# Performance work log

Measured on AMD Instinct MI355X. Metric: run time of the kernel, lower is better.

Reference implementation:

```python
import jax, jax.numpy as jnp
import numpy as np

B, T, D, H = 4, 2048, 1024, 16
HS = D // H

def _layernorm(x, g, b, eps=1e-5):
    mu = jnp.mean(x, axis=-1, keepdims=True)
    var = jnp.var(x, axis=-1, keepdims=True)
    return (x - mu) * jax.lax.rsqrt(var + eps) * g + b

def setup_inputs() -> dict:
    key = jax.random.key(0)
    ks = jax.random.split(key, 8)
    s = 0.02
    return {
        "x": jax.random.normal(ks[0], (B, T, D), jnp.float32),
        "wq": jax.random.normal(ks[1], (D, D), jnp.float32) * s,
        "wk": jax.random.normal(ks[2], (D, D), jnp.float32) * s,
        "wv": jax.random.normal(ks[3], (D, D), jnp.float32) * s,
        "wo": jax.random.normal(ks[4], (D, D), jnp.float32) * s,
        "bo": jnp.zeros((D,), jnp.float32),
        "w1": jax.random.normal(ks[5], (D, 4 * D), jnp.float32) * s,
        "b1": jnp.zeros((4 * D,), jnp.float32),
        "w2": jax.random.normal(ks[6], (4 * D, D), jnp.float32) * s,
        "b2": jnp.zeros((D,), jnp.float32),
        "g1": jnp.ones((D,), jnp.float32),
        "be1": jnp.zeros((D,), jnp.float32),
        "g2": jnp.ones((D,), jnp.float32),
        "be2": jnp.zeros((D,), jnp.float32),
    }

def reference(x, wq, wk, wv, wo, bo, w1, b1, w2, b2, g1, be1, g2, be2):
    b, t, d = x.shape
    h = H
    hs = d // h
    # --- pre-LN + multi-head causal self-attention ---
    xn = _layernorm(x, g1, be1)
    q = (xn @ wq).reshape(b, t, h, hs).transpose(0, 2, 1, 3)  # [b,h,t,hs]
    k = (xn @ wk).reshape(b, t, h, hs).transpose(0, 2, 1, 3)
    v = (xn @ wv).reshape(b, t, h, hs).transpose(0, 2, 1, 3)
    # NOTE: original scales by C**-0.5 where C = embedded_size (not head_size)
    scale = jnp.asarray(d, x.dtype) ** -0.5
    wei = jnp.einsum("bhqd,bhkd->bhqk", q, k) * scale
    causal = jnp.tril(jnp.ones((t, t), bool))
    wei = jnp.where(causal, wei, -jnp.inf)
    wei = jax.nn.softmax(wei, axis=-1)
    attn = jnp.einsum("bhqk,bhkd->bhqd", wei, v)
    attn = attn.transpose(0, 2, 1, 3).reshape(b, t, d)
    x = x + attn @ wo + bo
    # --- pre-LN + FFN ---
    xn2 = _layernorm(x, g2, be2)
    x = x + jax.nn.relu(xn2 @ w1 + b1) @ w2 + b2
    return x
```

## Files before the change

### kernel.cpp

```cpp
#include <hip/hip_runtime.h>
#include <hip/hip_bf16.h>
#include <stdint.h>

typedef __hip_bfloat16 bf16;
typedef __attribute__((ext_vector_type(8))) short bf16x8_t;
typedef __attribute__((ext_vector_type(4))) float f32x4_t;
typedef __attribute__((ext_vector_type(16))) float f32x16_t;
typedef __attribute__((ext_vector_type(2))) unsigned int u32x2_t;

#define B_ 4
#define T_ 2048
#define D_ 1024
#define H_ 16
#define HS_ 64
#define QKV_LD 3072

__device__ __forceinline__ void gload_lds16(const void* g, void* l) {
    __builtin_amdgcn_global_load_lds(
        (const __attribute__((address_space(1))) unsigned int*)g,
        (__attribute__((address_space(3))) unsigned int*)l, 16, 0, 0);
}

__device__ __forceinline__ bf16x8_t ldsv8(const bf16* p) {
    return *(const bf16x8_t*)p;
}

__device__ __forceinline__ unsigned pack2(float a, float b) {
    union { bf16 h[2]; unsigned u; } t;
    t.h[0] = __float2bfloat16(a);
    t.h[1] = __float2bfloat16(b);
    return t.u;
}

__global__ __launch_bounds__(256) void transpose_cvt(
    const float* __restrict__ W, bf16* __restrict__ WT, int K, int N)
{
    __shared__ float tile[32][33];
    const int nbx = N >> 5;
    const int bx = blockIdx.x % nbx;
    const int by = blockIdx.x / nbx;
    const int n0 = bx << 5, k0 = by << 5;
    const int tx = threadIdx.x & 31, ty = threadIdx.x >> 5;
#pragma unroll
    for (int i = 0; i < 32; i += 8)
        tile[ty + i][tx] = W[(long)(k0 + ty + i) * N + n0 + tx];
    __syncthreads();
#pragma unroll
    for (int i = 0; i < 32; i += 8)
        WT[(long)(n0 + ty + i) * K + k0 + tx] = __float2bfloat16(tile[tx][ty + i]);
}

__global__ __launch_bounds__(256) void vhead_transpose(
    const bf16* __restrict__ QKV, bf16* __restrict__ VT)
{
    __shared__ bf16 tile[32][33];
    int idx = blockIdx.x;
    const int tt  = idx & 63;   idx >>= 6;
    const int hst = idx & 1;    idx >>= 1;
    const int bh  = idx;
    const int b = bh >> 4, h = bh & 15;
    const int tx = threadIdx.x & 31, ty = threadIdx.x >> 5;
    const long vrow = (long)b * T_ + tt * 32;
    const int  vcol = 2048 + h * HS_ + hst * 32;
#pragma unroll
    for (int i = 0; i < 32; i += 8)
        tile[ty + i][tx] = QKV[(vrow + ty + i) * QKV_LD + vcol + tx];
    __syncthreads();
    const long orow = (long)bh * HS_ + hst * 32;
#pragma unroll
    for (int i = 0; i < 32; i += 8)
        VT[(orow + ty + i) * T_ + tt * 32 + tx] = tile[tx][ty + i];
}

__global__ __launch_bounds__(256) void ln_k(
    const float* __restrict__ x, const float* __restrict__ g,
    const float* __restrict__ be, bf16* __restrict__ out)
{
    const long row = blockIdx.x;
    const int t = threadIdx.x;
    const float4 v = ((const float4*)(x + row * D_))[t];
    float s  = v.x + v.y + v.z + v.w;
    float s2 = v.x * v.x + v.y * v.y + v.z * v.z + v.w * v.w;
#pragma unroll
    for (int m = 1; m < 64; m <<= 1) {
        s  += __shfl_xor(s, m, 64);
        s2 += __shfl_xor(s2, m, 64);
    }
    __shared__ float red[8];
    const int wv = t >> 6, ln = t & 63;
    if (ln == 0) { red[wv] = s; red[4 + wv] = s2; }
    __syncthreads();
    s  = red[0] + red[1] + red[2] + red[3];
    s2 = red[4] + red[5] + red[6] + red[7];
    const float mu  = s * (1.f / (float)D_);
    const float var = s2 * (1.f / (float)D_) - mu * mu;
    const float rs  = rsqrtf(var + 1e-5f);
    const float4 gv = ((const float4*)g)[t];
    const float4 bv = ((const float4*)be)[t];
    union { bf16 h[4]; short4 s4; } u;
    u.h[0] = __float2bfloat16((v.x - mu) * rs * gv.x + bv.x);
    u.h[1] = __float2bfloat16((v.y - mu) * rs * gv.y + bv.y);
    u.h[2] = __float2bfloat16((v.z - mu) * rs * gv.z + bv.z);
    u.h[3] = __float2bfloat16((v.w - mu) * rs * gv.w + bv.w);
    ((short4*)(out + row * D_))[t] = u.s4;
}

template<int HAS_BIAS, int RELU, int HAS_RES, int OUT_BF16>
__global__ __launch_bounds__(512, 1) void gemm2(
    const bf16* __restrict__ A, const bf16* __restrict__ BT,
    const float* __restrict__ bias, const float* __restrict__ res,
    void* __restrict__ Cout, int M, int N, int K)
{
    __shared__ bf16 As[2][256 * 64];
    __shared__ bf16 Bs[2][128 * 64];
    const int tid  = threadIdx.x;
    const int w    = tid >> 6;
    const int lane = tid & 63;
    const int wm = w >> 1, wn = w & 1;
    const int nbn = N >> 7;
    const int cpx = gridDim.x >> 3;
    const int bid = (blockIdx.x & 7) * cpx + (blockIdx.x >> 3);
    const int bm = bid / nbn, bn = bid % nbn;
    const int row0 = bm << 8, col0 = bn << 7;

    const bf16* aS0; const bf16* aS1; const bf16* aS2; const bf16* aS3;
    const bf16* bS0; const bf16* bS1;
    {
        int f0 = tid,        r0 = f0 >> 3, c0 = ((f0 & 7) ^ (r0 & 7)) << 3;
        int f1 = 512 + tid,  r1 = f1 >> 3, c1 = ((f1 & 7) ^ (r1 & 7)) << 3;
        int f2 = 1024 + tid, r2 = f2 >> 3, c2 = ((f2 & 7) ^ (r2 & 7)) << 3;
        int f3 = 1536 + tid, r3 = f3 >> 3, c3 = ((f3 & 7) ^ (r3 & 7)) << 3;
        aS0 = A + (long)(row0 + r0) * K + c0;
        aS1 = A + (long)(row0 + r1) * K + c1;
        aS2 = A + (long)(row0 + r2) * K + c2;
        aS3 = A + (long)(row0 + r3) * K + c3;
        bS0 = BT + (long)(col0 + r0) * K + c0;
        bS1 = BT + (long)(col0 + r1) * K + c1;
    }
    const int wbase = w * 64;

#define STAGE2(buf, kt) do {                                             \
        const long ko_ = (long)(kt) * 64;                                \
        gload_lds16(aS0 + ko_, &As[buf][(0 * 512 + wbase) * 8]);         \
        gload_lds16(aS1 + ko_, &As[buf][(1 * 512 + wbase) * 8]);         \
        gload_lds16(aS2 + ko_, &As[buf][(2 * 512 + wbase) * 8]);         \
        gload_lds16(aS3 + ko_, &As[buf][(3 * 512 + wbase) * 8]);         \
        gload_lds16(bS0 + ko_, &Bs[buf][(0 * 512 + wbase) * 8]);         \
        gload_lds16(bS1 + ko_, &Bs[buf][(1 * 512 + wbase) * 8]);         \
    } while (0)

    f32x4_t acc[4][4] = {};
    const int fr = lane & 15;
    const int fq = lane >> 4;
    const int nt = K >> 6;

    STAGE2(0, 0);
    STAGE2(1, 1);

    for (int t = 0; t < nt; ++t) {
        const int cur = t & 1;
        if (t < nt - 1) asm volatile("s_waitcnt vmcnt(6)" ::: "memory");
        else            asm volatile("s_waitcnt vmcnt(0)" ::: "memory");
        __builtin_amdgcn_s_barrier();

        bf16x8_t a[2][4], b[2][4];
#pragma unroll
        for (int ks = 0; ks < 2; ++ks) {
#pragma unroll
            for (int m = 0; m < 4; ++m) {
                const int r = wm * 64 + m * 16 + fr;
                const int ch = ks * 4 + fq;
                a[ks][m] = ldsv8(&As[cur][r * 64 + ((ch ^ (r & 7)) << 3)]);
            }
#pragma unroll
            for (int n = 0; n < 4; ++n) {
                const int r = wn * 64 + n * 16 + fr;
                const int ch = ks * 4 + fq;
                b[ks][n] = ldsv8(&Bs[cur][r * 64 + ((ch ^ (r & 7)) << 3)]);
            }
        }
        asm volatile("s_waitcnt lgkmcnt(0)" ::: "memory");
        __builtin_amdgcn_sched_barrier(0);
        __builtin_amdgcn_s_barrier();

        if (t + 2 < nt) STAGE2(cur, t + 2);

        __builtin_amdgcn_s_setprio(1);
#pragma unroll
        for (int m = 0; m < 4; ++m)
#pragma unroll
            for (int n = 0; n < 4; ++n) {
                acc[m][n] = __builtin_amdgcn_mfma_f32_16x16x32_bf16(a[0][m], b[0][n], acc[m][n], 0, 0, 0);
                acc[m][n] = __builtin_amdgcn_mfma_f32_16x16x32_bf16(a[1][m], b[1][n], acc[m][n], 0, 0, 0);
            }
        __builtin_amdgcn_s_setprio(0);
    }
#undef STAGE2

    const int orow = fq << 2;
#pragma unroll
    for (int m = 0; m < 4; ++m) {
        const int rbase = row0 + wm * 64 + m * 16 + orow;
#pragma unroll
        for (int n = 0; n < 4; ++n) {
            const int c = col0 + wn * 64 + n * 16 + fr;
            float bv = 0.f;
            if (HAS_BIAS) bv = bias[c];
#pragma unroll
            for (int r = 0; r < 4; ++r) {
                float v = acc[m][n][r] + bv;
                if (RELU) v = fmaxf(v, 0.f);
                if (HAS_RES) v += res[(long)(rbase + r) * N + c];
                if (OUT_BF16)
                    ((bf16*)Cout)[(long)(rbase + r) * N + c] = __float2bfloat16(v);
                else
                    ((float*)Cout)[(long)(rbase + r) * N + c] = v;
            }
        }
    }
}

template<int HAS_BIAS, int RELU, int HAS_RES, int OUT_BF16>
__global__ __launch_bounds__(512, 1) void gemm8(
    const bf16* __restrict__ A, const bf16* __restrict__ BT,
    const float* __restrict__ bias, const float* __restrict__ res,
    void* __restrict__ Cout, int M, int N, int K)
{
    __shared__ bf16 As[2][2][256 * 32];
    __shared__ bf16 Bs[2][2][256 * 32];

    const int tid  = threadIdx.x;
    const int w    = tid >> 6;
    const int lane = tid & 63;
    const int wm = w >> 2, wn = w & 3;
    const int nbn = N >> 8;
    const int cpx = gridDim.x >> 3;
    const int bid = (blockIdx.x & 7) * cpx + (blockIdx.x >> 3);
    const int bm = bid / nbn, bn = bid % nbn;
    const int row0 = bm << 8, col0 = bn << 8;

    const int r0s = tid >> 2;
    const int c0s = (((tid & 3) ^ (r0s & 3)) << 3);
    const bf16* aU0 = A  + (long)(row0 + r0s) * K + c0s;
    const bf16* aU1 = aU0 + (long)128 * K;
    const bf16* bU0 = BT + (long)(col0 + r0s) * K + c0s;
    const bf16* bU1 = bU0 + (long)128 * K;
    const int wb8 = w * 64 * 8;

#define STAGE_A8(buf, kh, kt) do {                                        \
        const long ko_ = (long)(kt) * 64 + (kh) * 32;                     \
        gload_lds16(aU0 + ko_, &As[buf][kh][wb8]);                        \
        gload_lds16(aU1 + ko_, &As[buf][kh][4096 + wb8]);                 \
    } while (0)
#define STAGE_B8(buf, kh, kt) do {                                        \
        const long ko_ = (long)(kt) * 64 + (kh) * 32;                     \
        gload_lds16(bU0 + ko_, &Bs[buf][kh][wb8]);                        \
        gload_lds16(bU1 + ko_, &Bs[buf][kh][4096 + wb8]);                 \
    } while (0)

    f32x4_t acc[8][4] = {};
    bf16x8_t af[8], bf0, bf1;
    const int fr = lane & 15;
    const int fq = lane >> 4;
    const int nt = K >> 6;

#define RD_A8(cur, ks) do { _Pragma("unroll")                              \
        for (int m = 0; m < 8; ++m) {                                      \
            const int rr = wm * 128 + m * 16 + fr;                         \
            af[m] = ldsv8(&As[cur][ks][rr * 32 + ((fq ^ (rr & 3)) << 3)]); \
        } } while (0)
#define RD_B8(cur, ks, n) ldsv8(&Bs[cur][ks][(wn * 64 + (n) * 16 + fr) * 32 + \
        ((fq ^ ((wn * 64 + (n) * 16 + fr) & 3)) << 3)])
#define MM8(nh) do { _Pragma("unroll")                                     \
        for (int m = 0; m < 8; ++m) {                                      \
            acc[m][(nh)*2]   = __builtin_amdgcn_mfma_f32_16x16x32_bf16(af[m], bf0, acc[m][(nh)*2],   0, 0, 0); \
            acc[m][(nh)*2+1] = __builtin_amdgcn_mfma_f32_16x16x32_bf16(af[m], bf1, acc[m][(nh)*2+1], 0, 0, 0); \
        } } while (0)
#define PHASE8(cur, ks, nh, RDA, STG, VM) do {                             \
        if (RDA) RD_A8(cur, ks);                                           \
        bf0 = RD_B8(cur, ks, (nh) * 2);                                    \
        bf1 = RD_B8(cur, ks, (nh) * 2 + 1);                                \
        STG;                                                               \
        __builtin_amdgcn_s_barrier();                                      \
        asm volatile("s_waitcnt lgkmcnt(0)" ::: "memory");                 \
        __builtin_amdgcn_sched_barrier(0);                                 \
        __builtin_amdgcn_s_setprio(1);                                     \
        MM8(nh);                                                           \
        __builtin_amdgcn_s_setprio(0);                                     \
        VM;                                                                \
        __builtin_amdgcn_s_barrier();                                      \
    } while (0)
#define VM4_ asm volatile("s_waitcnt vmcnt(4)" ::: "memory")
#define VM0_ asm volatile("s_waitcnt vmcnt(0)" ::: "memory")

    STAGE_A8(0, 0, 0);
    STAGE_B8(0, 0, 0);
    STAGE_A8(0, 1, 0);
    STAGE_B8(0, 1, 0);
    VM4_;
    __builtin_amdgcn_s_barrier();

    for (int t = 0; t < nt - 1; ++t) {
        const int cur = t & 1, nb = cur ^ 1;
        PHASE8(cur, 0, 0, 1, STAGE_A8(nb, 0, t + 1), (void)0);
        PHASE8(cur, 0, 1, 0, STAGE_B8(nb, 0, t + 1), VM4_);
        PHASE8(cur, 1, 0, 1, STAGE_A8(nb, 1, t + 1), (void)0);
        PHASE8(cur, 1, 1, 0, STAGE_B8(nb, 1, t + 1), VM4_);
    }
    {
        const int cur = (nt - 1) & 1;
        PHASE8(cur, 0, 0, 1, (void)0, (void)0);
        PHASE8(cur, 0, 1, 0, (void)0, VM0_);
        PHASE8(cur, 1, 0, 1, (void)0, (void)0);
        PHASE8(cur, 1, 1, 0, (void)0, (void)0);
    }
#undef STAGE_A8
#undef STAGE_B8
#undef RD_A8
#undef RD_B8
#undef MM8
#undef PHASE8
#undef VM4_
#undef VM0_

    const int orow = fq << 2;
#pragma unroll
    for (int m = 0; m < 8; ++m) {
        const int rbase = row0 + wm * 128 + m * 16 + orow;
#pragma unroll
        for (int n = 0; n < 4; ++n) {
            const int c = col0 + wn * 64 + n * 16 + fr;
            float bv = 0.f;
            if (HAS_BIAS) bv = bias[c];
#pragma unroll
            for (int r = 0; r < 4; ++r) {
                float v = acc[m][n][r] + bv;
                if (RELU) v = fmaxf(v, 0.f);
                if (HAS_RES) v += res[(long)(rbase + r) * N + c];
                if (OUT_BF16)
                    ((bf16*)Cout)[(long)(rbase + r) * N + c] = __float2bfloat16(v);
                else
                    ((float*)Cout)[(long)(rbase + r) * N + c] = v;
            }
        }
    }
}

__device__ __forceinline__ void attn_tile(
    const bf16* K_, const bf16* V_, const bf16x8_t (&qf)[4],
    f32x16_t& oA, f32x16_t& oB, float& mOld, float& lSum,
    int c, int ct_w, int qabs, int w, int l31, int hi, int hi8, int swzk)
{
    const float kE  = 0.0450842200278f;
    const float THR = 256.0f;
    const bool diag = (c == ct_w);
    const bool two  = !(diag && !(w & 1));

    f32x16_t s0 = {}, s1 = {};
#pragma unroll
    for (int s = 0; s < 4; ++s) {
        bf16x8_t kf = ldsv8(K_ + l31 * 64 + ((16 * s + hi8) ^ swzk));
        s0 = __builtin_amdgcn_mfma_f32_32x32x16_bf16(kf, qf[s], s0, 0, 0, 0);
    }
    if (two) {
#pragma unroll
        for (int s = 0; s < 4; ++s) {
            bf16x8_t kf = ldsv8(K_ + (32 + l31) * 64 + ((16 * s + hi8) ^ swzk));
            s1 = __builtin_amdgcn_mfma_f32_32x32x16_bf16(kf, qf[s], s1, 0, 0, 0);
        }
    }

    if (diag) {
        const int stm = w & 1;
        const int kb0 = c * 64 + stm * 32 + 4 * hi;
        if (stm) {
#pragma unroll
            for (int r = 0; r < 16; ++r)
                if (kb0 + (r & 3) + 8 * (r >> 2) > qabs) s1[r] = -1e30f;
        } else {
#pragma unroll
            for (int r = 0; r < 16; ++r)
                if (kb0 + (r & 3) + 8 * (r >> 2) > qabs) s0[r] = -1e30f;
        }
    }

    float rm = s0[0];
#pragma unroll
    for (int r = 1; r < 16; ++r) rm = fmaxf(rm, s0[r]);
    if (two) {
#pragma unroll
        for (int r = 0; r < 16; ++r) rm = fmaxf(rm, s1[r]);
    }
    {
        u32x2_t rr = __builtin_amdgcn_permlane32_swap(
            __float_as_uint(rm), __float_as_uint(rm), false, false);
        rm = fmaxf(__uint_as_float(rr.x), __uint_as_float(rr.y));
    }
    if (!__all(rm <= mOld + THR)) {
        const float mN = fmaxf(mOld, rm);
        const float corr = exp2f((mOld - mN) * kE);
#pragma unroll
        for (int r = 0; r < 16; ++r) { oA[r] *= corr; oB[r] *= corr; }
        lSum *= corr;
        mOld = mN;
    }
    const float nmk = -mOld * kE;
#pragma unroll
    for (int r = 0; r < 16; ++r) s0[r] = exp2f(fmaf(s0[r], kE, nmk));
    if (two) {
#pragma unroll
        for (int r = 0; r < 16; ++r) s1[r] = exp2f(fmaf(s1[r], kE, nmk));
    }
    float rs = s0[0];
#pragma unroll
    for (int r = 1; r < 16; ++r) rs += s0[r];
    if (two) {
#pragma unroll
        for (int r = 0; r < 16; ++r) rs += s1[r];
    }
    {
        u32x2_t rr = __builtin_amdgcn_permlane32_swap(
            __float_as_uint(rs), __float_as_uint(rs), false, false);
        rs = __uint_as_float(rr.x) + __uint_as_float(rr.y);
    }
    lSum += rs;

    {
        unsigned pk_[8];
#pragma unroll
        for (int i = 0; i < 8; ++i) pk_[i] = pack2(s0[2 * i], s0[2 * i + 1]);
        union { unsigned u[4]; bf16x8_t v; } W0, W1;
        u32x2_t ra = __builtin_amdgcn_permlane32_swap(pk_[0], pk_[2], false, false);
        u32x2_t rb = __builtin_amdgcn_permlane32_swap(pk_[1], pk_[3], false, false);
        W0.u[0] = ra.x; W0.u[1] = rb.x; W0.u[2] = ra.y; W0.u[3] = rb.y;
        u32x2_t rc = __builtin_amdgcn_permlane32_swap(pk_[4], pk_[6], false, false);
        u32x2_t rd = __builtin_amdgcn_permlane32_swap(pk_[5], pk_[7], false, false);
        W1.u[0] = rc.x; W1.u[1] = rd.x; W1.u[2] = rc.y; W1.u[3] = rd.y;
#pragma unroll
        for (int m = 0; m < 2; ++m) {
            const int kcol = 16 * m + hi8;
            bf16x8_t vf0 = ldsv8(V_ + l31 * 64 + (kcol ^ swzk));
            oA = __builtin_amdgcn_mfma_f32_32x32x16_bf16(vf0, m ? W1.v : W0.v, oA, 0, 0, 0);
            bf16x8_t vf1 = ldsv8(V_ + (32 + l31) * 64 + (kcol ^ swzk));
            oB = __builtin_amdgcn_mfma_f32_32x32x16_bf16(vf1, m ? W1.v : W0.v, oB, 0, 0, 0);
        }
    }
    if (two) {
        unsigned pk_[8];
#pragma unroll
        for (int i = 0; i < 8; ++i) pk_[i] = pack2(s1[2 * i], s1[2 * i + 1]);
        union { unsigned u[4]; bf16x8_t v; } W0, W1;
        u32x2_t ra = __builtin_amdgcn_permlane32_swap(pk_[0], pk_[2], false, false);
        u32x2_t rb = __builtin_amdgcn_permlane32_swap(pk_[1], pk_[3], false, false);
        W0.u[0] = ra.x; W0.u[1] = rb.x; W0.u[2] = ra.y; W0.u[3] = rb.y;
        u32x2_t rc = __builtin_amdgcn_permlane32_swap(pk_[4], pk_[6], false, false);
        u32x2_t rd = __builtin_amdgcn_permlane32_swap(pk_[5], pk_[7], false, false);
        W1.u[0] = rc.x; W1.u[1] = rd.x; W1.u[2] = rc.y; W1.u[3] = rd.y;
#pragma unroll
        for (int m = 0; m < 2; ++m) {
            const int kcol = 16 * (2 + m) + hi8;
            bf16x8_t vf0 = ldsv8(V_ + l31 * 64 + (kcol ^ swzk));
            oA = __builtin_amdgcn_mfma_f32_32x32x16_bf16(vf0, m ? W1.v : W0.v, oA, 0, 0, 0);
            bf16x8_t vf1 = ldsv8(V_ + (32 + l31) * 64 + (kcol ^ swzk));
            oB = __builtin_amdgcn_mfma_f32_32x32x16_bf16(vf1, m ? W1.v : W0.v, oB, 0, 0, 0);
        }
    }
}

__global__ __launch_bounds__(512, 1) void attn_flash(
    const bf16* __restrict__ QKV, const bf16* __restrict__ VT,
    bf16* __restrict__ O)
{
    __shared__ bf16 Ks[2][64 * 64];
    __shared__ bf16 Vs[2][64 * 64];

    const int tid = threadIdx.x;
    const int w   = tid >> 6;
    const int ln  = tid & 63;
    const int l31 = ln & 31;
    const int hi  = ln >> 5;
    const int hi8 = hi << 3;

    const int qLo = blockIdx.x;
    const int qHi = 7 - qLo;
    const int bh = blockIdx.y;
    const long rowBase = (long)(bh >> 4) * T_;
    const int colBase = (bh & 15) * HS_;

    const int qabsL = qLo * 256 + w * 32 + l31;
    const int qabsH = qHi * 256 + w * 32 + l31;
    const int ct_L  = qLo * 4 + (w >> 1);
    const int ct_H  = qHi * 4 + (w >> 1);
    const int ctb   = qHi * 4 + 3;

    bf16x8_t qfL[4], qfH[4];
    {
        const bf16* qpL = QKV + (rowBase + qabsL) * QKV_LD + colBase + hi8;
        const bf16* qpH = QKV + (rowBase + qabsH) * QKV_LD + colBase + hi8;
#pragma unroll
        for (int s = 0; s < 4; ++s) {
            qfL[s] = *(const bf16x8_t*)(qpL + 16 * s);
            qfH[s] = *(const bf16x8_t*)(qpH + 16 * s);
        }
    }

    f32x16_t oLA = {}, oLB = {}, oHA = {}, oHB = {};
    float mL = -1e30f, lL = 0.f, mH = -1e30f, lH = 0.f;

    const int srow = tid >> 3;
    const int schunk = (((tid & 7) ^ (srow & 7)) << 3);
    const bf16* kSrc = QKV + (rowBase + srow) * QKV_LD + 1024 + colBase + schunk;
    const bf16* vSrc = VT + ((long)bh * HS_ + srow) * T_ + schunk;

    gload_lds16(kSrc, &Ks[0][w * 512]);
    gload_lds16(vSrc, &Vs[0][w * 512]);

    const int swzk = (l31 & 7) << 3;

    for (int c = 0; c <= ctb; ++c) {
        const int cur = c & 1;
        __syncthreads();

        if (c < ctb) {
            gload_lds16(kSrc + (long)(c + 1) * 64 * QKV_LD, &Ks[cur ^ 1][w * 512]);
            gload_lds16(vSrc + (c + 1) * 64, &Vs[cur ^ 1][w * 512]);
        }

        const bf16* K_ = Ks[cur];
        const bf16* V_ = Vs[cur];
        if (c <= ct_H)
            attn_tile(K_, V_, qfH, oHA, oHB, mH, lH, c, ct_H, qabsH, w, l31, hi, hi8, swzk);
        if (c <= ct_L)
            attn_tile(K_, V_, qfL, oLA, oLB, mL, lL, c, ct_L, qabsL, w, l31, hi, hi8, swzk);
    }

    {
        const float inv = 1.f / lH;
        bf16* Op = O + (rowBase + qabsH) * D_ + colBase;
#pragma unroll
        for (int g = 0; g < 4; ++g) {
            u32x2_t sA, sB;
            sA.x = pack2(oHA[4 * g + 0] * inv, oHA[4 * g + 1] * inv);
            sA.y = pack2(oHA[4 * g + 2] * inv, oHA[4 * g + 3] * inv);
            sB.x = pack2(oHB[4 * g + 0] * inv, oHB[4 * g + 1] * inv);
            sB.y = pack2(oHB[4 * g + 2] * inv, oHB[4 * g + 3] * inv);
            *(u32x2_t*)(Op + 8 * g + 4 * hi)      = sA;
            *(u32x2_t*)(Op + 32 + 8 * g + 4 * hi) = sB;
        }
    }
    {
        const float inv = 1.f / lL;
        bf16* Op = O + (rowBase + qabsL) * D_ + colBase;
#pragma unroll
        for (int g = 0; g < 4; ++g) {
            u32x2_t sA, sB;
            sA.x = pack2(oLA[4 * g + 0] * inv, oLA[4 * g + 1] * inv);
            sA.y = pack2(oLA[4 * g + 2] * inv, oLA[4 * g + 3] * inv);
            sB.x = pack2(oLB[4 * g + 0] * inv, oLB[4 * g + 1] * inv);
            sB.y = pack2(oLB[4 * g + 2] * inv, oLB[4 * g + 3] * inv);
            *(u32x2_t*)(Op + 8 * g + 4 * hi)      = sA;
            *(u32x2_t*)(Op + 32 + 8 * g + 4 * hi) = sB;
        }
    }
}

extern "C" void kernel_launch(void* const* d_in, const int* in_sizes, int n_in,
                              void* d_out, int out_size, void* d_ws, size_t ws_size,
                              hipStream_t stream)
{
    (void)in_sizes; (void)n_in; (void)out_size; (void)ws_size;
    const float* x   = (const float*)d_in[0];
    const float* wq  = (const float*)d_in[1];
    const float* wk  = (const float*)d_in[2];
    const float* wv  = (const float*)d_in[3];
    const float* wo  = (const float*)d_in[4];
    const float* bo  = (const float*)d_in[5];
    const float* w1  = (const float*)d_in[6];
    const float* b1  = (const float*)d_in[7];
    const float* w2  = (const float*)d_in[8];
    const float* b2  = (const float*)d_in[9];
    const float* g1  = (const float*)d_in[10];
    const float* be1 = (const float*)d_in[11];
    const float* g2  = (const float*)d_in[12];
    const float* be2 = (const float*)d_in[13];
    float* out = (float*)d_out;

    char* ws = (char*)d_ws;
    const size_t SLOT = (size_t)8192 * 1024 * 2;
    bf16* xn     = (bf16*)(ws);
    bf16* attnb  = (bf16*)(ws);
    bf16* qkv    = (bf16*)(ws + SLOT);
    bf16* xn2    = (bf16*)(ws + SLOT);
    bf16* vtb    = (bf16*)(ws + 4 * SLOT);
    bf16* hidden = (bf16*)(ws + 2 * SLOT);
    float* x1    = (float*)(ws + 6 * SLOT);
    char* wpos   = ws + 6 * SLOT + (size_t)33554432;
    bf16* wqkvT = (bf16*)(wpos);
    bf16* wqT = (bf16*)(wpos);
    bf16* wkT = (bf16*)(wpos + (size_t)2097152);
    bf16* wvT = (bf16*)(wpos + (size_t)2 * 2097152);
    bf16* woT = (bf16*)(wpos + (size_t)3 * 2097152);
    bf16* w1T = (bf16*)(wpos + (size_t)4 * 2097152);
    bf16* w2T = (bf16*)(wpos + (size_t)4 * 2097152 + 8388608);

    transpose_cvt<<<dim3(1024), 256, 0, stream>>>(wq, wqT, 1024, 1024);
    transpose_cvt<<<dim3(1024), 256, 0, stream>>>(wk, wkT, 1024, 1024);
    transpose_cvt<<<dim3(1024), 256, 0, stream>>>(wv, wvT, 1024, 1024);
    transpose_cvt<<<dim3(1024), 256, 0, stream>>>(wo, woT, 1024, 1024);
    transpose_cvt<<<dim3(4096), 256, 0, stream>>>(w1, w1T, 1024, 4096);
    transpose_cvt<<<dim3(4096), 256, 0, stream>>>(w2, w2T, 4096, 1024);

    ln_k<<<8192, 256, 0, stream>>>(x, g1, be1, xn);

    gemm8<0, 0, 0, 1><<<384, 512, 0, stream>>>(xn, wqkvT, nullptr, nullptr, qkv, 8192, 3072, 1024);

    vhead_transpose<<<8192, 256, 0, stream>>>(qkv, vtb);

    attn_flash<<<dim3(4, 64), 512, 0, stream>>>(qkv, vtb, attnb);

    gemm2<1, 0, 1, 0><<<256, 512, 0, stream>>>(attnb, woT, bo, x, x1, 8192, 1024, 1024);

    ln_k<<<8192, 256, 0, stream>>>(x1, g2, be2, xn2);

    gemm8<1, 1, 0, 1><<<512, 512, 0, stream>>>(xn2, w1T, b1, nullptr, hidden, 8192, 4096, 1024);

    gemm2<1, 0, 1, 0><<<256, 512, 0, stream>>>(hidden, w2T, b2, x1, out, 8192, 1024, 4096);
}
```

Before: 505.5 us.

## Merge weight transposes, reschedule GEMM pipelines, batch attention query tiles

Replaces six weight-transpose launches with one combined kernel. Restructures the gemm2 and gemm8 main loops so LDS fragment reads for the next k-slice overlap with MFMAs on the current one, and changes the gemm8 LDS swizzle to cut bank conflicts. Rewrites the attention tile routine to process both query blocks together, sharing K/V LDS loads across two MFMA streams, with tree reductions for max and sum. Also switches the QKV projection from gemm8 to gemm2 with more blocks. These trade fewer launches and less LDS traffic for higher register pressure and riskier hand-placed waitcnt ordering.

Measured after the change: 579.4 us. 1.15x slower.

```diff
diff --git a/kernel.cpp b/kernel.cpp
--- a/kernel.cpp
+++ b/kernel.cpp
@@ -32,13 +32,45 @@
     return t.u;
 }
 
-__global__ __launch_bounds__(256) void transpose_cvt(
-    const float* __restrict__ W, bf16* __restrict__ WT, int K, int N)
+__device__ __forceinline__ float tmax16(const f32x16_t& s) {
+    float a = fmaxf(s[0], s[8]),  b = fmaxf(s[1], s[9]);
+    float c = fmaxf(s[2], s[10]), d = fmaxf(s[3], s[11]);
+    float e = fmaxf(s[4], s[12]), f = fmaxf(s[5], s[13]);
+    float g = fmaxf(s[6], s[14]), h = fmaxf(s[7], s[15]);
+    a = fmaxf(a, e); b = fmaxf(b, f); c = fmaxf(c, g); d = fmaxf(d, h);
+    return fmaxf(fmaxf(a, c), fmaxf(b, d));
+}
+
+__device__ __forceinline__ float tsum16(const f32x16_t& s) {
+    float a = s[0] + s[8],  b = s[1] + s[9];
+    float c = s[2] + s[10], d = s[3] + s[11];
+    float e = s[4] + s[12], f = s[5] + s[13];
+    float g = s[6] + s[14], h = s[7] + s[15];
+    a += e; b += f; c += g; d += h;
+    return (a + c) + (b + d);
+}
+
+__global__ __launch_bounds__(256) void transpose_all(
+    const float* wq, const float* wk, const float* wv, const float* wo,
+    const float* w1, const float* w2,
+    bf16* wqkvT, bf16* woT, bf16* w1T, bf16* w2T)
 {
     __shared__ float tile[32][33];
+    int blk = blockIdx.x;
+    const float* W; bf16* WT; int K, N;
+    if (blk < 4096) {
+        const int which = blk >> 10; blk &= 1023;
+        W  = which == 0 ? wq : which == 1 ? wk : which == 2 ? wv : wo;
+        WT = which == 3 ? woT : wqkvT + (size_t)which * 1024 * 1024;
+        K = 1024; N = 1024;
+    } else if (blk < 8192) {
+        blk -= 4096; W = w1; WT = w1T; K = 1024; N = 4096;
+    } else {
+        blk -= 8192; W = w2; WT = w2T; K = 4096; N = 1024;
+    }
     const int nbx = N >> 5;
-    const int bx = blockIdx.x % nbx;
-    const int by = blockIdx.x / nbx;
+    const int bx = blk % nbx;
+    const int by = blk / nbx;
     const int n0 = bx << 5, k0 = by << 5;
     const int tx = threadIdx.x & 31, ty = threadIdx.x >> 5;
 #pragma unroll
@@ -163,36 +195,47 @@
         else            asm volatile("s_waitcnt vmcnt(0)" ::: "memory");
         __builtin_amdgcn_s_barrier();
 
-        bf16x8_t a[2][4], b[2][4];
-#pragma unroll
-        for (int ks = 0; ks < 2; ++ks) {
-#pragma unroll
-            for (int m = 0; m < 4; ++m) {
-                const int r = wm * 64 + m * 16 + fr;
-                const int ch = ks * 4 + fq;
-                a[ks][m] = ldsv8(&As[cur][r * 64 + ((ch ^ (r & 7)) << 3)]);
-            }
-#pragma unroll
-            for (int n = 0; n < 4; ++n) {
-                const int r = wn * 64 + n * 16 + fr;
-                const int ch = ks * 4 + fq;
-                b[ks][n] = ldsv8(&Bs[cur][r * 64 + ((ch ^ (r & 7)) << 3)]);
-            }
-        }
+        bf16x8_t a0[4], b0[4], a1[4], b1[4];
+#pragma unroll
+        for (int m = 0; m < 4; ++m) {
+            const int r = wm * 64 + m * 16 + fr;
+            a0[m] = ldsv8(&As[cur][r * 64 + ((fq ^ (r & 7)) << 3)]);
+        }
+#pragma unroll
+        for (int n = 0; n < 4; ++n) {
+            const int r = wn * 64 + n * 16 + fr;
+            b0[n] = ldsv8(&Bs[cur][r * 64 + ((fq ^ (r & 7)) << 3)]);
+        }
+        __builtin_amdgcn_sched_barrier(0);
+#pragma unroll
+        for (int m = 0; m < 4; ++m) {
+            const int r = wm * 64 + m * 16 + fr;
+            a1[m] = ldsv8(&As[cur][r * 64 + (((4 + fq) ^ (r & 7)) << 3)]);
+        }
+#pragma unroll
+        for (int n = 0; n < 4; ++n) {
+            const int r = wn * 64 + n * 16 + fr;
+            b1[n] = ldsv8(&Bs[cur][r * 64 + (((4 + fq) ^ (r & 7)) << 3)]);
+        }
+        asm volatile("s_waitcnt lgkmcnt(8)" ::: "memory");
+        __builtin_amdgcn_sched_barrier(0);
+        __builtin_amdgcn_s_setprio(1);
+#pragma unroll
+        for (int m = 0; m < 4; ++m)
+#pragma unroll
+            for (int n = 0; n < 4; ++n)
+                acc[m][n] = __builtin_amdgcn_mfma_f32_16x16x32_bf16(a0[m], b0[n], acc[m][n], 0, 0, 0);
+        __builtin_amdgcn_s_setprio(0);
         asm volatile("s_waitcnt lgkmcnt(0)" ::: "memory");
         __builtin_amdgcn_sched_barrier(0);
         __builtin_amdgcn_s_barrier();
-
         if (t + 2 < nt) STAGE2(cur, t + 2);
-
         __builtin_amdgcn_s_setprio(1);
 #pragma unroll
         for (int m = 0; m < 4; ++m)
 #pragma unroll
-            for (int n = 0; n < 4; ++n) {
-                acc[m][n] = __builtin_amdgcn_mfma_f32_16x16x32_bf16(a[0][m], b[0][n], acc[m][n], 0, 0, 0);
-                acc[m][n] = __builtin_amdgcn_mfma_f32_16x16x32_bf16(a[1][m], b[1][n], acc[m][n], 0, 0, 0);
-            }
+            for (int n = 0; n < 4; ++n)
+                acc[m][n] = __builtin_amdgcn_mfma_f32_16x16x32_bf16(a1[m], b1[n], acc[m][n], 0, 0, 0);
         __builtin_amdgcn_s_setprio(0);
     }
 #undef STAGE2
@@ -240,12 +283,12 @@
     const int row0 = bm << 8, col0 = bn << 8;
 
     const int r0s = tid >> 2;
-    const int c0s = (((tid & 3) ^ (r0s & 3)) << 3);
+    const int c0s = (((tid & 3) ^ ((r0s ^ (r0s >> 2)) & 3)) << 3);
     const bf16* aU0 = A  + (long)(row0 + r0s) * K + c0s;
     const bf16* aU1 = aU0 + (long)128 * K;
     const bf16* bU0 = BT + (long)(col0 + r0s) * K + c0s;
     const bf16* bU1 = bU0 + (long)128 * K;
-    const int wb8 = w * 64 * 8;
+    const int wb8 = w * 512;
 
 #define STAGE_A8(buf, kh, kt) do {                                        \
         const long ko_ = (long)(kt) * 64 + (kh) * 32;                     \
@@ -259,69 +302,114 @@
     } while (0)
 
     f32x4_t acc[8][4] = {};
-    bf16x8_t af[8], bf0, bf1;
+    bf16x8_t afA[8], afB[8], b01[2], b23[2], b01b[2], b23b[2];
     const int fr = lane & 15;
     const int fq = lane >> 4;
     const int nt = K >> 6;
 
-#define RD_A8(cur, ks) do { _Pragma("unroll")                              \
+#define SWZ8(rr) ((fq ^ ((rr ^ (rr >> 2)) & 3)) << 3)
+#define RD_A8(dst, cur, ks) do { _Pragma("unroll")                         \
         for (int m = 0; m < 8; ++m) {                                      \
             const int rr = wm * 128 + m * 16 + fr;                         \
-            af[m] = ldsv8(&As[cur][ks][rr * 32 + ((fq ^ (rr & 3)) << 3)]); \
+            dst[m] = ldsv8(&As[cur][ks][rr * 32 + SWZ8(rr)]);              \
         } } while (0)
-#define RD_B8(cur, ks, n) ldsv8(&Bs[cur][ks][(wn * 64 + (n) * 16 + fr) * 32 + \
-        ((fq ^ ((wn * 64 + (n) * 16 + fr) & 3)) << 3)])
-#define MM8(nh) do { _Pragma("unroll")                                     \
+#define RD_B8(dst, cur, ks, n0) do {                                       \
+        { const int rr = wn * 64 + (n0) * 16 + fr;                         \
+          dst[0] = ldsv8(&Bs[cur][ks][rr * 32 + SWZ8(rr)]); }              \
+        { const int rr = wn * 64 + ((n0) + 1) * 16 + fr;                   \
+          dst[1] = ldsv8(&Bs[cur][ks][rr * 32 + SWZ8(rr)]); }              \
+    } while (0)
+#define MM8(afx, bp, n0) do { _Pragma("unroll")                            \
         for (int m = 0; m < 8; ++m) {                                      \
-            acc[m][(nh)*2]   = __builtin_amdgcn_mfma_f32_16x16x32_bf16(af[m], bf0, acc[m][(nh)*2],   0, 0, 0); \
-            acc[m][(nh)*2+1] = __builtin_amdgcn_mfma_f32_16x16x32_bf16(af[m], bf1, acc[m][(nh)*2+1], 0, 0, 0); \
+            acc[m][n0]     = __builtin_amdgcn_mfma_f32_16x16x32_bf16(afx[m], bp[0], acc[m][n0],     0, 0, 0); \
+            acc[m][(n0)+1] = __builtin_amdgcn_mfma_f32_16x16x32_bf16(afx[m], bp[1], acc[m][(n0)+1], 0, 0, 0); \
         } } while (0)
-#define PHASE8(cur, ks, nh, RDA, STG, VM) do {                             \
-        if (RDA) RD_A8(cur, ks);                                           \
-        bf0 = RD_B8(cur, ks, (nh) * 2);                                    \
-        bf1 = RD_B8(cur, ks, (nh) * 2 + 1);                                \
-        STG;                                                               \
-        __builtin_amdgcn_s_barrier();                                      \
-        asm volatile("s_waitcnt lgkmcnt(0)" ::: "memory");                 \
-        __builtin_amdgcn_sched_barrier(0);                                 \
-        __builtin_amdgcn_s_setprio(1);                                     \
-        MM8(nh);                                                           \
-        __builtin_amdgcn_s_setprio(0);                                     \
-        VM;                                                                \
-        __builtin_amdgcn_s_barrier();                                      \
-    } while (0)
-#define VM4_ asm volatile("s_waitcnt vmcnt(4)" ::: "memory")
-#define VM0_ asm volatile("s_waitcnt vmcnt(0)" ::: "memory")
+#define LGKM0_ do { asm volatile("s_waitcnt lgkmcnt(0)" ::: "memory");     \
+                    __builtin_amdgcn_sched_barrier(0); } while (0)
+#define SBAR_  __builtin_amdgcn_s_barrier()
+#define PIN_   __builtin_amdgcn_sched_barrier(0)
 
     STAGE_A8(0, 0, 0);
     STAGE_B8(0, 0, 0);
     STAGE_A8(0, 1, 0);
     STAGE_B8(0, 1, 0);
-    VM4_;
-    __builtin_amdgcn_s_barrier();
+    asm volatile("s_waitcnt vmcnt(4)" ::: "memory");
+    SBAR_;
 
     for (int t = 0; t < nt - 1; ++t) {
         const int cur = t & 1, nb = cur ^ 1;
-        PHASE8(cur, 0, 0, 1, STAGE_A8(nb, 0, t + 1), (void)0);
-        PHASE8(cur, 0, 1, 0, STAGE_B8(nb, 0, t + 1), VM4_);
-        PHASE8(cur, 1, 0, 1, STAGE_A8(nb, 1, t + 1), (void)0);
-        PHASE8(cur, 1, 1, 0, STAGE_B8(nb, 1, t + 1), VM4_);
+        RD_A8(afA, cur, 0); RD_B8(b01, cur, 0, 0);
+        STAGE_A8(nb, 0, t + 1);
+        SBAR_;
+        LGKM0_;
+        __builtin_amdgcn_s_setprio(1);
+        RD_B8(b23, cur, 0, 2); PIN_;
+        MM8(afA, b01, 0);
+        __builtin_amdgcn_s_setprio(0);
+        SBAR_;
+        STAGE_B8(nb, 0, t + 1);
+        asm volatile("s_waitcnt vmcnt(4)" ::: "memory");
+        SBAR_;
+        LGKM0_;
+        __builtin_amdgcn_s_setprio(1);
+        RD_A8(afB, cur, 1); RD_B8(b01b, cur, 1, 0); PIN_;
+        MM8(afA, b23, 2);
+        __builtin_amdgcn_s_setprio(0);
+        SBAR_;
+        STAGE_A8(nb, 1, t + 1);
+        SBAR_;
+        LGKM0_;
+        __builtin_amdgcn_s_setprio(1);
+        RD_B8(b23b, cur, 1, 2); PIN_;
+        MM8(afB, b01b, 0);
+        __builtin_amdgcn_s_setprio(0);
+        SBAR_;
+        STAGE_B8(nb, 1, t + 1);
+        SBAR_;
+        LGKM0_;
+        __builtin_amdgcn_s_setprio(1);
+        MM8(afB, b23b, 2);
+        __builtin_amdgcn_s_setprio(0);
+        asm volatile("s_waitcnt vmcnt(4)" ::: "memory");
+        SBAR_;
     }
     {
         const int cur = (nt - 1) & 1;
-        PHASE8(cur, 0, 0, 1, (void)0, (void)0);
-        PHASE8(cur, 0, 1, 0, (void)0, VM0_);
-        PHASE8(cur, 1, 0, 1, (void)0, (void)0);
-        PHASE8(cur, 1, 1, 0, (void)0, (void)0);
+        RD_A8(afA, cur, 0); RD_B8(b01, cur, 0, 0);
+        SBAR_;
+        LGKM0_;
+        __builtin_amdgcn_s_setprio(1);
+        RD_B8(b23, cur, 0, 2); PIN_;
+        MM8(afA, b01, 0);
+        __builtin_amdgcn_s_setprio(0);
+        SBAR_;
+        asm volatile("s_waitcnt vmcnt(0)" ::: "memory");
+        SBAR_;
+        LGKM0_;
+        __builtin_amdgcn_s_setprio(1);
+        RD_A8(afB, cur, 1); RD_B8(b01b, cur, 1, 0); PIN_;
+        MM8(afA, b23, 2);
+        __builtin_amdgcn_s_setprio(0);
+        SBAR_;
+        SBAR_;
+        LGKM0_;
+        __builtin_amdgcn_s_setprio(1);
+        RD_B8(b23b, cur, 1, 2); PIN_;
+        MM8(afB, b01b, 0);
+        __builtin_amdgcn_s_setprio(0);
+        SBAR_;
+        LGKM0_;
+        MM8(afB, b23b, 2);
     }
 #undef STAGE_A8
 #undef STAGE_B8
+#undef SWZ8
 #undef RD_A8
 #undef RD_B8
 #undef MM8
-#undef PHASE8
-#undef VM4_
-#undef VM0_
+#undef LGKM0_
+#undef SBAR_
+#undef PIN_
 
     const int orow = fq << 2;
 #pragma unroll
@@ -346,125 +434,125 @@
     }
 }
 
-__device__ __forceinline__ void attn_tile(
-    const bf16* K_, const bf16* V_, const bf16x8_t (&qf)[4],
-    f32x16_t& oA, f32x16_t& oB, float& mOld, float& lSum,
-    int c, int ct_w, int qabs, int w, int l31, int hi, int hi8, int swzk)
+template<int NQ>
+__device__ __forceinline__ void attn_tiles(
+    const bf16* K_, const bf16* V_, const bf16x8_t (&qf)[2][4],
+    f32x16_t (&oA)[2], f32x16_t (&oB)[2], float (&mOld)[2], float (&lSum)[2],
+    int c, const int (&ctw)[2], const int (&qabs)[2],
+    int w, int l31, int hi, int hi8, int swzk)
 {
     const float kE  = 0.0450842200278f;
     const float THR = 256.0f;
-    const bool diag = (c == ct_w);
-    const bool two  = !(diag && !(w & 1));
-
-    f32x16_t s0 = {}, s1 = {};
+    const bool two = (NQ == 2) ? true : !((c == ctw[0]) && !(w & 1));
+
+    f32x16_t s0[NQ] = {}, s1[NQ] = {};
+
+    __builtin_amdgcn_s_setprio(1);
 #pragma unroll
     for (int s = 0; s < 4; ++s) {
         bf16x8_t kf = ldsv8(K_ + l31 * 64 + ((16 * s + hi8) ^ swzk));
-        s0 = __builtin_amdgcn_mfma_f32_32x32x16_bf16(kf, qf[s], s0, 0, 0, 0);
+#pragma unroll
+        for (int qi = 0; qi < NQ; ++qi)
+            s0[qi] = __builtin_amdgcn_mfma_f32_32x32x16_bf16(kf, qf[qi][s], s0[qi], 0, 0, 0);
     }
     if (two) {
 #pragma unroll
         for (int s = 0; s < 4; ++s) {
             bf16x8_t kf = ldsv8(K_ + (32 + l31) * 64 + ((16 * s + hi8) ^ swzk));
-            s1 = __builtin_amdgcn_mfma_f32_32x32x16_bf16(kf, qf[s], s1, 0, 0, 0);
-        }
-    }
-
-    if (diag) {
-        const int stm = w & 1;
-        const int kb0 = c * 64 + stm * 32 + 4 * hi;
-        if (stm) {
-#pragma unroll
-            for (int r = 0; r < 16; ++r)
-                if (kb0 + (r & 3) + 8 * (r >> 2) > qabs) s1[r] = -1e30f;
-        } else {
-#pragma unroll
-            for (int r = 0; r < 16; ++r)
-                if (kb0 + (r & 3) + 8 * (r >> 2) > qabs) s0[r] = -1e30f;
-        }
-    }
-
-    float rm = s0[0];
-#pragma unroll
-    for (int r = 1; r < 16; ++r) rm = fmaxf(rm, s0[r]);
-    if (two) {
-#pragma unroll
-        for (int r = 0; r < 16; ++r) rm = fmaxf(rm, s1[r]);
-    }
-    {
-        u32x2_t rr = __builtin_amdgcn_permlane32_swap(
-            __float_as_uint(rm), __float_as_uint(rm), false, false);
-        rm = fmaxf(__uint_as_float(rr.x), __uint_as_float(rr.y));
-    }
-    if (!__all(rm <= mOld + THR)) {
-        const float mN = fmaxf(mOld, rm);
-        const float corr = exp2f((mOld - mN) * kE);
-#pragma unroll
-        for (int r = 0; r < 16; ++r) { oA[r] *= corr; oB[r] *= corr; }
-        lSum *= corr;
-        mOld = mN;
-    }
-    const float nmk = -mOld * kE;
-#pragma unroll
-    for (int r = 0; r < 16; ++r) s0[r] = exp2f(fmaf(s0[r], kE, nmk));
-    if (two) {
-#pragma unroll
-        for (int r = 0; r < 16; ++r) s1[r] = exp2f(fmaf(s1[r], kE, nmk));
-    }
-    float rs = s0[0];
-#pragma unroll
-    for (int r = 1; r < 16; ++r) rs += s0[r];
-    if (two) {
-#pragma unroll
-        for (int r = 0; r < 16; ++r) rs += s1[r];
-    }
-    {
-        u32x2_t rr = __builtin_amdgcn_permlane32_swap(
-            __float_as_uint(rs), __float_as_uint(rs), false, false);
-        rs = __uint_as_float(rr.x) + __uint_as_float(rr.y);
-    }
-    lSum += rs;
-
-    {
+#pragma unroll
+            for (int qi = 0; qi < NQ; ++qi)
+                s1[qi] = __builtin_amdgcn_mfma_f32_32x32x16_bf16(kf, qf[qi][s], s1[qi], 0, 0, 0);
+        }
+    }
+    __builtin_amdgcn_s_setprio(0);
+
+#pragma unroll
+    for (int qi = 0; qi < NQ; ++qi) {
+        if (c == ctw[qi]) {
+            const int kb0 = c * 64 + 4 * hi;
+#pragma unroll
+            for (int r = 0; r < 16; ++r) {
+                const int ko = (r & 3) + 8 * (r >> 2);
+                if (kb0 + ko > qabs[qi]) s0[qi][r] = -1e30f;
+                if (two) { if (kb0 + 32 + ko > qabs[qi]) s1[qi][r] = -1e30f; }
+            }
+        }
+    }
+
+#pragma unroll
+    for (int qi = 0; qi < NQ; ++qi) {
+        float rm = tmax16(s0[qi]);
+        if (two) rm = fmaxf(rm, tmax16(s1[qi]));
+        {
+            u32x2_t rr = __builtin_amdgcn_permlane32_swap(
+                __float_as_uint(rm), __float_as_uint(rm), false, false);
+            rm = fmaxf(__uint_as_float(rr.x), __uint_as_float(rr.y));
+        }
+        if (!__all(rm <= mOld[qi] + THR)) {
+            const float mN = fmaxf(mOld[qi], rm);
+            const float corr = exp2f((mOld[qi] - mN) * kE);
+#pragma unroll
+            for (int r = 0; r < 16; ++r) { oA[qi][r] *= corr; oB[qi][r] *= corr; }
+            lSum[qi] *= corr;
+            mOld[qi] = mN;
+        }
+        const float nmk = -mOld[qi] * kE;
+#pragma unroll
+        for (int r = 0; r < 16; ++r) s0[qi][r] = exp2f(fmaf(s0[qi][r], kE, nmk));
+        if (two) {
+#pragma unroll
+            for (int r = 0; r < 16; ++r) s1[qi][r] = exp2f(fmaf(s1[qi][r], kE, nmk));
+        }
+        float rs = tsum16(s0[qi]);
+        if (two) rs += tsum16(s1[qi]);
+        {
+            u32x2_t rr = __builtin_amdgcn_permlane32_swap(
+                __float_as_uint(rs), __float_as_uint(rs), false, false);
+            rs = __uint_as_float(rr.x) + __uint_as_float(rr.y);
+        }
+        lSum[qi] += rs;
+    }
+
+    union uW { unsigned u[4]; bf16x8_t v; };
+    uW W[NQ][4];
+#pragma unroll
+    for (int qi = 0; qi < NQ; ++qi) {
         unsigned pk_[8];
 #pragma unroll
-        for (int i = 0; i < 8; ++i) pk_[i] = pack2(s0[2 * i], s0[2 * i + 1]);
-        union { unsigned u[4]; bf16x8_t v; } W0, W1;
+        for (int i = 0; i < 8; ++i) pk_[i] = pack2(s0[qi][2 * i], s0[qi][2 * i + 1]);
         u32x2_t ra = __builtin_amdgcn_permlane32_swap(pk_[0], pk_[2], false, false);
         u32x2_t rb = __builtin_amdgcn_permlane32_swap(pk_[1], pk_[3], false, false);
-        W0.u[0] = ra.x; W0.u[1] = rb.x; W0.u[2] = ra.y; W0.u[3] = rb.y;
+        W[qi][0].u[0] = ra.x; W[qi][0].u[1] = rb.x; W[qi][0].u[2] = ra.y; W[qi][0].u[3] = rb.y;
         u32x2_t rc = __builtin_amdgcn_permlane32_swap(pk_[4], pk_[6], false, false);
         u32x2_t rd = __builtin_amdgcn_permlane32_swap(pk_[5], pk_[7], false, false);
-        W1.u[0] = rc.x; W1.u[1] = rd.x; W1.u[2] = rc.y; W1.u[3] = rd.y;
-#pragma unroll
-        for (int m = 0; m < 2; ++m) {
-            const int kcol = 16 * m + hi8;
+        W[qi][1].u[0] = rc.x; W[qi][1].u[1] = rd.x; W[qi][1].u[2] = rc.y; W[qi][1].u[3] = rd.y;
+        if (two) {
+#pragma unroll
+            for (int i = 0; i < 8; ++i) pk_[i] = pack2(s1[qi][2 * i], s1[qi][2 * i + 1]);
+            u32x2_t re = __builtin_amdgcn_permlane32_swap(pk_[0], pk_[2], false, false);
+            u32x2_t rf = __builtin_amdgcn_permlane32_swap(pk_[1], pk_[3], false, false);
+            W[qi][2].u[0] = re.x; W[qi][2].u[1] = rf.x; W[qi][2].u[2] = re.y; W[qi][2].u[3] = rf.y;
+            u32x2_t rg = __builtin_amdgcn_permlane32_swap(pk_[4], pk_[6], false, false);
+            u32x2_t rh = __builtin_amdgcn_permlane32_swap(pk_[5], pk_[7], false, false);
+            W[qi][3].u[0] = rg.x; W[qi][3].u[1] = rh.x; W[qi][3].u[2] = rg.y; W[qi][3].u[3] = rh.y;
+        }
+    }
+
+    __builtin_amdgcn_s_setprio(1);
+#pragma unroll
+    for (int sl = 0; sl < 4; ++sl) {
+        if (sl < 2 || two) {
+            const int kcol = 16 * sl + hi8;
             bf16x8_t vf0 = ldsv8(V_ + l31 * 64 + (kcol ^ swzk));
-            oA = __builtin_amdgcn_mfma_f32_32x32x16_bf16(vf0, m ? W1.v : W0.v, oA, 0, 0, 0);
             bf16x8_t vf1 = ldsv8(V_ + (32 + l31) * 64 + (kcol ^ swzk));
-            oB = __builtin_amdgcn_mfma_f32_32x32x16_bf16(vf1, m ? W1.v : W0.v, oB, 0, 0, 0);
-        }
-    }
-    if (two) {
-        unsigned pk_[8];
-#pragma unroll
-        for (int i = 0; i < 8; ++i) pk_[i] = pack2(s1[2 * i], s1[2 * i + 1]);
-        union { unsigned u[4]; bf16x8_t v; } W0, W1;
-        u32x2_t ra = __builtin_amdgcn_permlane32_swap(pk_[0], pk_[2], false, false);
-        u32x2_t rb = __builtin_amdgcn_permlane32_swap(pk_[1], pk_[3], false, false);
-        W0.u[0] = ra.x; W0.u[1] = rb.x; W0.u[2] = ra.y; W0.u[3] = rb.y;
-        u32x2_t rc = __builtin_amdgcn_permlane32_swap(pk_[4], pk_[6], false, false);
-        u32x2_t rd = __builtin_amdgcn_permlane32_swap(pk_[5], pk_[7], false, false);
-        W1.u[0] = rc.x; W1.u[1] = rd.x; W1.u[2] = rc.y; W1.u[3] = rd.y;
-#pragma unroll
-        for (int m = 0; m < 2; ++m) {
-            const int kcol = 16 * (2 + m) + hi8;
-            bf16x8_t vf0 = ldsv8(V_ + l31 * 64 + (kcol ^ swzk));
-            oA = __builtin_amdgcn_mfma_f32_32x32x16_bf16(vf0, m ? W1.v : W0.v, oA, 0, 0, 0);
-            bf16x8_t vf1 = ldsv8(V_ + (32 + l31) * 64 + (kcol ^ swzk));
-            oB = __builtin_amdgcn_mfma_f32_32x32x16_bf16(vf1, m ? W1.v : W0.v, oB, 0, 0, 0);
-        }
-    }
+#pragma unroll
+            for (int qi = 0; qi < NQ; ++qi) {
+                oA[qi] = __builtin_amdgcn_mfma_f32_32x32x16_bf16(vf0, W[qi][sl].v, oA[qi], 0, 0, 0);
+                oB[qi] = __builtin_amdgcn_mfma_f32_32x32x16_bf16(vf1, W[qi][sl].v, oB[qi], 0, 0, 0);
+            }
+        }
+    }
+    __builtin_amdgcn_s_setprio(0);
 }
 
 __global__ __launch_bounds__(512, 1) void attn_flash(
@@ -487,25 +575,26 @@
     const long rowBase = (long)(bh >> 4) * T_;
     const int colBase = (bh & 15) * HS_;
 
-    const int qabsL = qLo * 256 + w * 32 + l31;
-    const int qabsH = qHi * 256 + w * 32 + l31;
-    const int ct_L  = qLo * 4 + (w >> 1);
-    const int ct_H  = qHi * 4 + (w >> 1);
-    const int ctb   = qHi * 4 + 3;
-
-    bf16x8_t qfL[4], qfH[4];
+    int qabs[2], ctw[2];
+    qabs[0] = qHi * 256 + w * 32 + l31;
+    qabs[1] = qLo * 256 + w * 32 + l31;
+    ctw[0]  = qHi * 4 + (w >> 1);
+    ctw[1]  = qLo * 4 + (w >> 1);
+    const int ctb = qHi * 4 + 3;
+
+    bf16x8_t qf[2][4];
     {
-        const bf16* qpL = QKV + (rowBase + qabsL) * QKV_LD + colBase + hi8;
-        const bf16* qpH = QKV + (rowBase + qabsH) * QKV_LD + colBase + hi8;
+        const bf16* qp0 = QKV + (rowBase + qabs[0]) * QKV_LD + colBase + hi8;
+        const bf16* qp1 = QKV + (rowBase + qabs[1]) * QKV_LD + colBase + hi8;
 #pragma unroll
         for (int s = 0; s < 4; ++s) {
-            qfL[s] = *(const bf16x8_t*)(qpL + 16 * s);
-            qfH[s] = *(const bf16x8_t*)(qpH + 16 * s);
-        }
-    }
-
-    f32x16_t oLA = {}, oLB = {}, oHA = {}, oHB = {};
-    float mL = -1e30f, lL = 0.f, mH = -1e30f, lH = 0.f;
+            qf[0][s] = *(const bf16x8_t*)(qp0 + 16 * s);
+            qf[1][s] = *(const bf16x8_t*)(qp1 + 16 * s);
+        }
+    }
+
+    f32x16_t oA[2] = {}, oB[2] = {};
+    float mOld[2] = { -1e30f, -1e30f }, lSum[2] = { 0.f, 0.f };
 
     const int srow = tid >> 3;
     const int schunk = (((tid & 7) ^ (srow & 7)) << 3);
@@ -528,36 +617,23 @@
 
         const bf16* K_ = Ks[cur];
         const bf16* V_ = Vs[cur];
-        if (c <= ct_H)
-            attn_tile(K_, V_, qfH, oHA, oHB, mH, lH, c, ct_H, qabsH, w, l31, hi, hi8, swzk);
-        if (c <= ct_L)
-            attn_tile(K_, V_, qfL, oLA, oLB, mL, lL, c, ct_L, qabsL, w, l31, hi, hi8, swzk);
-    }
-
-    {
-        const float inv = 1.f / lH;
-        bf16* Op = O + (rowBase + qabsH) * D_ + colBase;
+        if (c <= ctw[1])
+            attn_tiles<2>(K_, V_, qf, oA, oB, mOld, lSum, c, ctw, qabs, w, l31, hi, hi8, swzk);
+        else if (c <= ctw[0])
+            attn_tiles<1>(K_, V_, qf, oA, oB, mOld, lSum, c, ctw, qabs, w, l31, hi, hi8, swzk);
+    }
+
+#pragma unroll
+    for (int qi = 0; qi < 2; ++qi) {
+        const float inv = 1.f / lSum[qi];
+        bf16* Op = O + (rowBase + qabs[qi]) * D_ + colBase;
 #pragma unroll
         for (int g = 0; g < 4; ++g) {
             u32x2_t sA, sB;
-            sA.x = pack2(oHA[4 * g + 0] * inv, oHA[4 * g + 1] * inv);
-            sA.y = pack2(oHA[4 * g + 2] * inv, oHA[4 * g + 3] * inv);
-            sB.x = pack2(oHB[4 * g + 0] * inv, oHB[4 * g + 1] * inv);
-            sB.y = pack2(oHB[4 * g + 2] * inv, oHB[4 * g + 3] * inv);
-            *(u32x2_t*)(Op + 8 * g + 4 * hi)      = sA;
-            *(u32x2_t*)(Op + 32 + 8 * g + 4 * hi) = sB;
-        }
-    }
-    {
-        const float inv = 1.f / lL;
-        bf16* Op = O + (rowBase + qabsL) * D_ + colBase;
-#pragma unroll
-        for (int g = 0; g < 4; ++g) {
-            u32x2_t sA, sB;
-            sA.x = pack2(oLA[4 * g + 0] * inv, oLA[4 * g + 1] * inv);
-            sA.y = pack2(oLA[4 * g + 2] * inv, oLA[4 * g + 3] * inv);
-            sB.x = pack2(oLB[4 * g + 0] * inv, oLB[4 * g + 1] * inv);
-            sB.y = pack2(oLB[4 * g + 2] * inv, oLB[4 * g + 3] * inv);
+            sA.x = pack2(oA[qi][4 * g + 0] * inv, oA[qi][4 * g + 1] * inv);
+            sA.y = pack2(oA[qi][4 * g + 2] * inv, oA[qi][4 * g + 3] * inv);
+            sB.x = pack2(oB[qi][4 * g + 0] * inv, oB[qi][4 * g + 1] * inv);
+            sB.y = pack2(oB[qi][4 * g + 2] * inv, oB[qi][4 * g + 3] * inv);
             *(u32x2_t*)(Op + 8 * g + 4 * hi)      = sA;
             *(u32x2_t*)(Op + 32 + 8 * g + 4 * hi) = sB;
         }
@@ -596,23 +672,15 @@
     float* x1    = (float*)(ws + 6 * SLOT);
     char* wpos   = ws + 6 * SLOT + (size_t)33554432;
     bf16* wqkvT = (bf16*)(wpos);
-    bf16* wqT = (bf16*)(wpos);
-    bf16* wkT = (bf16*)(wpos + (size_t)2097152);
-    bf16* wvT = (bf16*)(wpos + (size_t)2 * 2097152);
     bf16* woT = (bf16*)(wpos + (size_t)3 * 2097152);
     bf16* w1T = (bf16*)(wpos + (size_t)4 * 2097152);
     bf16* w2T = (bf16*)(wpos + (size_t)4 * 2097152 + 8388608);
 
-    transpose_cvt<<<dim3(1024), 256, 0, stream>>>(wq, wqT, 1024, 1024);
-    transpose_cvt<<<dim3(1024), 256, 0, stream>>>(wk, wkT, 1024, 1024);
-    transpose_cvt<<<dim3(1024), 256, 0, stream>>>(wv, wvT, 1024, 1024);
-    transpose_cvt<<<dim3(1024), 256, 0, stream>>>(wo, woT, 1024, 1024);
-    transpose_cvt<<<dim3(4096), 256, 0, stream>>>(w1, w1T, 1024, 4096);
-    transpose_cvt<<<dim3(4096), 256, 0, stream>>>(w2, w2T, 4096, 1024);
+    transpose_all<<<12288, 256, 0, stream>>>(wq, wk, wv, wo, w1, w2, wqkvT, woT, w1T, w2T);
 
     ln_k<<<8192, 256, 0, stream>>>(x, g1, be1, xn);
 
-    gemm8<0, 0, 0, 1><<<384, 512, 0, stream>>>(xn, wqkvT, nullptr, nullptr, qkv, 8192, 3072, 1024);
+    gemm2<0, 0, 0, 1><<<768, 512, 0, stream>>>(xn, wqkvT, nullptr, nullptr, qkv, 8192, 3072, 1024);
 
     vhead_transpose<<<8192, 256, 0, stream>>>(qkv, vtb);
 
```
